# Kernel tuning notes

Hardware: AMD Instinct MI355X
Metric: run time of the kernel (lower is better)

Reference implementation:

```python
import jax, jax.numpy as jnp
import numpy as np

N, M = 4096, 8192
IN_DIM, OUT_DIM = 4096, 1024
NUM_SAMPLE = 10


def setup_inputs() -> dict:
    key = jax.random.key(0)
    k1, k2, k3, k4, k5 = jax.random.split(key, 5)
    node_features = jax.random.normal(k1, (N, IN_DIM), dtype=jnp.float32)
    neighbor_features = jax.random.normal(k2, (M, IN_DIM), dtype=jnp.float32)
    # Xavier-ish scale for params
    weight = jax.random.normal(k3, (OUT_DIM, IN_DIM), dtype=jnp.float32) * (1.0 / np.sqrt(IN_DIM))
    attention_vector = jax.random.normal(k4, (2 * OUT_DIM, 1), dtype=jnp.float32) * 0.05
    neighbor_idx = jax.random.randint(k5, (N, NUM_SAMPLE), 0, M, dtype=jnp.int32)
    return {
        "node_features": node_features,
        "neighbor_features": neighbor_features,
        "weight": weight,
        "attention_vector": attention_vector,
        "neighbor_idx": neighbor_idx,
    }


def reference(node_features, neighbor_features, weight, attention_vector, neighbor_idx):
    # Linear transform: [N, out], [M, out]
    node_t = node_features @ weight.T
    neigh_t = neighbor_features @ weight.T

    # combined @ attention_vector decomposes:
    # cat([h_i, h_j]) @ a == h_i @ a1 + h_j @ a2  (same math, no [N,M,2*out] tensor)
    a1 = attention_vector[:OUT_DIM, 0]   # [out]
    a2 = attention_vector[OUT_DIM:, 0]   # [out]
    scores = jax.nn.leaky_relu((node_t @ a1)[:, None] + (neigh_t @ a2)[None, :],
                               negative_slope=0.2)  # [N, M]

    # Build dense 0/1 mask from sampled neighbor indices (ragged -> dense)
    rows = jnp.arange(N, dtype=jnp.int32)[:, None]                  # [N,1]
    mask = jnp.zeros((N, M), dtype=jnp.float32).at[rows, neighbor_idx].set(1.0)

    scores = jnp.where(mask == 0, -jnp.inf, scores)
    attn = jax.nn.softmax(scores, axis=1)           # masked softmax over neighbor pool
    return attn @ neigh_t                           # [N, out]
```

## Files before the change

### kernel.cpp

```cpp
#include <hip/hip_runtime.h>

#define IN_DIM  4096
#define OUT_DIM 1024
#define NN      4096
#define MM      8192
#define NSAMP   10

typedef __bf16 bf16x8 __attribute__((ext_vector_type(8)));
typedef float  fx4    __attribute__((ext_vector_type(4)));

__device__ __forceinline__ ushort f2bf(float f) {
    union { float f; unsigned u; } v; v.f = f;
    unsigned u = v.u;
    return (ushort)((u + 0x7FFFu + ((u >> 16) & 1u)) >> 16);
}
__device__ __forceinline__ float bf2f(ushort u) {
    union { unsigned u; float f; } v; v.u = ((unsigned)u) << 16;
    return v.f;
}

#define GLDS(g, l) __builtin_amdgcn_global_load_lds(                           \
    (const __attribute__((address_space(1))) unsigned*)(g),                    \
    (__attribute__((address_space(3))) unsigned*)(l), 16, 0, 0)

__global__ __launch_bounds__(256) void k_attvec(const float* __restrict__ W,
                                                const float* __restrict__ att,
                                                float* __restrict__ v1,
                                                float* __restrict__ v2,
                                                ushort* __restrict__ Wbf) {
    int k  = blockIdx.x * 256 + threadIdx.x;
    int o0 = blockIdx.y * 32;
    float s1 = 0.f, s2 = 0.f;
    for (int o = o0; o < o0 + 32; ++o) {
        float w = W[(size_t)o * IN_DIM + k];
        Wbf[(size_t)o * IN_DIM + k] = f2bf(w);
        s1 += att[o] * w;
        s2 += att[OUT_DIM + o] * w;
    }
    atomicAdd(&v1[k], s1);
    atomicAdd(&v2[k], s2);
}

__global__ __launch_bounds__(256) void k_rows(const float* __restrict__ node_f,
                                              const float* __restrict__ neigh_f,
                                              const float* __restrict__ v1,
                                              const float* __restrict__ v2,
                                              float* __restrict__ nalpha,
                                              float* __restrict__ nbeta,
                                              ushort* __restrict__ Abf) {
    int row  = blockIdx.x * 4 + (threadIdx.x >> 6);
    int lane = threadIdx.x & 63;
    float s = 0.f;
    if (row < NN) {
        const float4* xr = reinterpret_cast<const float4*>(node_f + (size_t)row * IN_DIM);
        const float4* vr = reinterpret_cast<const float4*>(v1);
#pragma unroll
        for (int i = lane; i < IN_DIM / 4; i += 64) {
            float4 a = xr[i], b = vr[i];
            s += a.x * b.x + a.y * b.y + a.z * b.z + a.w * b.w;
        }
    } else {
        int j = row - NN;
        const float4* xr = reinterpret_cast<const float4*>(neigh_f + (size_t)j * IN_DIM);
        const float4* vr = reinterpret_cast<const float4*>(v2);
        ushort4* yr = reinterpret_cast<ushort4*>(Abf + (size_t)j * IN_DIM);
#pragma unroll
        for (int i = lane; i < IN_DIM / 4; i += 64) {
            float4 a = xr[i], b = vr[i];
            s += a.x * b.x + a.y * b.y + a.z * b.z + a.w * b.w;
            ushort4 o;
            o.x = f2bf(a.x); o.y = f2bf(a.y); o.z = f2bf(a.z); o.w = f2bf(a.w);
            yr[i] = o;
        }
    }
#pragma unroll
    for (int off = 32; off > 0; off >>= 1) s += __shfl_down(s, off, 64);
    if (lane == 0) {
        if (row < NN) nalpha[row] = s; else nbeta[row - NN] = s;
    }
}

#define BMT 256
#define BNT 256
#define BKG 32
#define KSPLIT (IN_DIM / 2)
#define NT (KSPLIT / BKG)

__device__ __forceinline__ void tile_compute(const ushort* __restrict__ as,
                                             const ushort* __restrict__ bs,
                                             int aoff, int boff,
                                             fx4 (&acc)[8][4]) {
    bf16x8 af[8], bfr[4];
#pragma unroll
    for (int mi = 0; mi < 8; ++mi)
        af[mi] = *reinterpret_cast<const bf16x8*>(as + aoff + mi * 512);
#pragma unroll
    for (int ni = 0; ni < 4; ++ni)
        bfr[ni] = *reinterpret_cast<const bf16x8*>(bs + boff + ni * 512);
    __builtin_amdgcn_s_setprio(1);
#pragma unroll
    for (int mi = 0; mi < 8; ++mi)
#pragma unroll
        for (int ni = 0; ni < 4; ++ni)
            acc[mi][ni] = __builtin_amdgcn_mfma_f32_16x16x32_bf16(af[mi], bfr[ni], acc[mi][ni], 0, 0, 0);
    __builtin_amdgcn_s_setprio(0);
}

__global__ __launch_bounds__(512, 2) void k_gemm(const ushort* __restrict__ A,
                                                 const ushort* __restrict__ B,
                                                 ushort* __restrict__ P) {
    __shared__ __align__(16) ushort As[4][BMT * BKG];
    __shared__ __align__(16) ushort Bs[4][BNT * BKG];

    const int tid  = threadIdx.x;
    const int lane = tid & 63;
    const int wid  = tid >> 6;
    const int wr   = wid >> 2;
    const int wc   = wid & 3;
    const int lrow = lane & 15;
    const int q    = lane >> 4;

    const int bid = blockIdx.x;
    const int swz = (bid & 7) * 32 + (bid >> 3);
    const int tx  = swz & 31;
    const int ty  = (swz >> 5) & 3;
    const int tz  = swz >> 7;
    const int bm  = tx * BMT;
    const int bn  = ty * BNT;
    const int kb  = tz * KSPLIT;

    const int sr  = tid >> 2;
    const int scu = (((tid & 3) ^ (sr & 3)) << 3);
    const ushort* gA0 = A + (size_t)(bm + sr) * IN_DIM + kb + scu;
    const ushort* gA1 = gA0 + (size_t)128 * IN_DIM;
    const ushort* gB0 = B + (size_t)(bn + sr) * IN_DIM + kb + scu;
    const ushort* gB1 = gB0 + (size_t)128 * IN_DIM;
    const int wbase = wid * 512;

#define STAGE(buf, kt) do {                                                    \
        GLDS(gA0 + (size_t)(kt) * BKG, &As[buf][0]        + wbase);            \
        GLDS(gA1 + (size_t)(kt) * BKG, &As[buf][0] + 4096 + wbase);            \
        GLDS(gB0 + (size_t)(kt) * BKG, &Bs[buf][0]        + wbase);            \
        GLDS(gB1 + (size_t)(kt) * BKG, &Bs[buf][0] + 4096 + wbase);            \
    } while (0)

    const int qs   = ((q ^ (lrow & 3)) << 3);
    const int aoff = (wr * 128 + lrow) * BKG + qs;
    const int boff = (wc * 64  + lrow) * BKG + qs;

    fx4 acc[8][4] = {};

    STAGE(0, 0); STAGE(1, 1); STAGE(2, 2);
    asm volatile("s_waitcnt vmcnt(8)" ::: "memory");
    __builtin_amdgcn_s_barrier();

    for (int t = 0; t < NT - 3; ++t) {
        STAGE((t + 3) & 3, t + 3);
        tile_compute(&As[t & 3][0], &Bs[t & 3][0], aoff, boff, acc);
        asm volatile("s_waitcnt vmcnt(8)" ::: "memory");
        __builtin_amdgcn_s_barrier();
    }
    tile_compute(&As[(NT - 3) & 3][0], &Bs[(NT - 3) & 3][0], aoff, boff, acc);
    asm volatile("s_waitcnt vmcnt(4)" ::: "memory");
    __builtin_amdgcn_s_barrier();
    tile_compute(&As[(NT - 2) & 3][0], &Bs[(NT - 2) & 3][0], aoff, boff, acc);
    asm volatile("s_waitcnt vmcnt(0)" ::: "memory");
    __builtin_amdgcn_s_barrier();
    tile_compute(&As[(NT - 1) & 3][0], &Bs[(NT - 1) & 3][0], aoff, boff, acc);
#undef STAGE

    ushort* Pz = P + (size_t)tz * MM * OUT_DIM;
#pragma unroll
    for (int mi = 0; mi < 8; ++mi)
#pragma unroll
        for (int ni = 0; ni < 4; ++ni) {
            int r = bm + wr * 128 + mi * 16 + q * 4;
            int c = bn + wc * 64  + ni * 16 + lrow;
#pragma unroll
            for (int v = 0; v < 4; ++v)
                Pz[(size_t)(r + v) * OUT_DIM + c] = f2bf(acc[mi][ni][v]);
        }
}

__global__ __launch_bounds__(256) void k_aggregate(const ushort* __restrict__ P,
                                                   const float* __restrict__ nalpha,
                                                   const float* __restrict__ nbeta,
                                                   const int* __restrict__ nidx,
                                                   float* __restrict__ outp) {
    int row = blockIdx.x;
    __shared__ int   s_idx[NSAMP];
    __shared__ float s_w[NSAMP];
    if (threadIdx.x < 16) {
        int t = threadIdx.x;
        int j = (t < NSAMP) ? nidx[row * NSAMP + t] : -1;
        float score = -INFINITY;
        if (t < NSAMP) {
            float x = nalpha[row] + nbeta[j];
            score = x > 0.f ? x : 0.2f * x;
        }
        bool dup = false;
#pragma unroll
        for (int sIdx = 0; sIdx < NSAMP; ++sIdx) {
            int js = __shfl(j, sIdx, 16);
            if (sIdx < t && js == j) dup = true;
        }
        float mx = score;
#pragma unroll
        for (int off = 8; off > 0; off >>= 1) {
            float o = __shfl_xor(mx, off, 16);
            mx = o > mx ? o : mx;
        }
        float e = (t < NSAMP && !dup) ? expf(score - mx) : 0.f;
        float sum = e;
#pragma unroll
        for (int off = 8; off > 0; off >>= 1) sum += __shfl_xor(sum, off, 16);
        if (t < NSAMP) {
            s_idx[t] = j;
            s_w[t]   = e / sum;
        }
    }
    __syncthreads();
    int col = threadIdx.x * 4;
    float ax = 0.f, ay = 0.f, az = 0.f, aw = 0.f;
#pragma unroll
    for (int t = 0; t < NSAMP; ++t) {
        float w = s_w[t];
        size_t off = (size_t)s_idx[t] * OUT_DIM + col;
        ushort4 u0 = *reinterpret_cast<const ushort4*>(P + off);
        ushort4 u1 = *reinterpret_cast<const ushort4*>(P + (size_t)MM * OUT_DIM + off);
        ax += w * (bf2f(u0.x) + bf2f(u1.x));
        ay += w * (bf2f(u0.y) + bf2f(u1.y));
        az += w * (bf2f(u0.z) + bf2f(u1.z));
        aw += w * (bf2f(u0.w) + bf2f(u1.w));
    }
    float4 o; o.x = ax; o.y = ay; o.z = az; o.w = aw;
    *reinterpret_cast<float4*>(outp + (size_t)row * OUT_DIM + col) = o;
}

extern "C" void kernel_launch(void* const* d_in, const int* in_sizes, int n_in,
                              void* d_out, int out_size, void* d_ws, size_t ws_size,
                              hipStream_t stream) {
    const float* node_f  = (const float*)d_in[0];
    const float* neigh_f = (const float*)d_in[1];
    const float* W       = (const float*)d_in[2];
    const float* att     = (const float*)d_in[3];
    const int*   nidx    = (const int*)d_in[4];
    float* outp = (float*)d_out;

    char* ws = (char*)d_ws;
    ushort* Abf = (ushort*)ws;
    ushort* Wbf = (ushort*)(ws + 67108864);
    ushort* P   = (ushort*)(ws + 75497472);
    float*  v1     = (float*)(ws + 109051904);
    float*  v2     = v1 + IN_DIM;
    float*  nalpha = v2 + IN_DIM;
    float*  nbeta  = nalpha + NN;

    hipMemsetAsync(v1, 0, 2 * IN_DIM * sizeof(float), stream);

    k_attvec   <<<dim3(16, 32),   256, 0, stream>>>(W, att, v1, v2, Wbf);
    k_rows     <<<(NN + MM) / 4,  256, 0, stream>>>(node_f, neigh_f, v1, v2, nalpha, nbeta, Abf);
    k_gemm     <<<256,            512, 0, stream>>>(Abf, Wbf, P);
    k_aggregate<<<NN,             256, 0, stream>>>(P, nalpha, nbeta, nidx, outp);
}
```

Measured before the change: 410.0 us.

## Restructure GEMM main loop into split-phase ping-pong with interleaved staging

The GEMM main loop now uses prefetch distance two instead of three. Each k-tile is split into two half-phases separated by barriers, and the A and B global-to-LDS loads for tile t+2 are interleaved with the MFMA halves. The LDS XOR swizzle changes to use bits 1-2 of the row, to cut bank conflicts on the fragment reads. k_attvec gets twice as many blocks, each with a 16-row unrolled loop, for more parallelism. The extra barriers and shallower prefetch could expose memory latency in exchange for lower register pressure and better overlap.

```diff
diff --git a/kernel.cpp b/kernel.cpp
--- a/kernel.cpp
+++ b/kernel.cpp
@@ -22,6 +22,8 @@
 #define GLDS(g, l) __builtin_amdgcn_global_load_lds(                           \
     (const __attribute__((address_space(1))) unsigned*)(g),                    \
     (__attribute__((address_space(3))) unsigned*)(l), 16, 0, 0)
+
+#define VMWAIT(N) asm volatile("s_waitcnt vmcnt(" #N ")" ::: "memory")
 
 __global__ __launch_bounds__(256) void k_attvec(const float* __restrict__ W,
                                                 const float* __restrict__ att,
@@ -29,9 +31,10 @@
                                                 float* __restrict__ v2,
                                                 ushort* __restrict__ Wbf) {
     int k  = blockIdx.x * 256 + threadIdx.x;
-    int o0 = blockIdx.y * 32;
+    int o0 = blockIdx.y * 16;
     float s1 = 0.f, s2 = 0.f;
-    for (int o = o0; o < o0 + 32; ++o) {
+#pragma unroll
+    for (int o = o0; o < o0 + 16; ++o) {
         float w = W[(size_t)o * IN_DIM + k];
         Wbf[(size_t)o * IN_DIM + k] = f2bf(w);
         s1 += att[o] * w;
@@ -86,25 +89,7 @@
 #define KSPLIT (IN_DIM / 2)
 #define NT (KSPLIT / BKG)
 
-__device__ __forceinline__ void tile_compute(const ushort* __restrict__ as,
-                                             const ushort* __restrict__ bs,
-                                             int aoff, int boff,
-                                             fx4 (&acc)[8][4]) {
-    bf16x8 af[8], bfr[4];
-#pragma unroll
-    for (int mi = 0; mi < 8; ++mi)
-        af[mi] = *reinterpret_cast<const bf16x8*>(as + aoff + mi * 512);
-#pragma unroll
-    for (int ni = 0; ni < 4; ++ni)
-        bfr[ni] = *reinterpret_cast<const bf16x8*>(bs + boff + ni * 512);
-    __builtin_amdgcn_s_setprio(1);
-#pragma unroll
-    for (int mi = 0; mi < 8; ++mi)
-#pragma unroll
-        for (int ni = 0; ni < 4; ++ni)
-            acc[mi][ni] = __builtin_amdgcn_mfma_f32_16x16x32_bf16(af[mi], bfr[ni], acc[mi][ni], 0, 0, 0);
-    __builtin_amdgcn_s_setprio(0);
-}
+#define MF(x, y, mi, ni) acc[mi][ni] = __builtin_amdgcn_mfma_f32_16x16x32_bf16((x), (y), acc[mi][ni], 0, 0, 0)
 
 __global__ __launch_bounds__(512, 2) void k_gemm(const ushort* __restrict__ A,
                                                  const ushort* __restrict__ B,
@@ -130,44 +115,88 @@
     const int kb  = tz * KSPLIT;
 
     const int sr  = tid >> 2;
-    const int scu = (((tid & 3) ^ (sr & 3)) << 3);
+    const int scu = (((tid & 3) ^ ((sr >> 1) & 3)) << 3);
     const ushort* gA0 = A + (size_t)(bm + sr) * IN_DIM + kb + scu;
     const ushort* gA1 = gA0 + (size_t)128 * IN_DIM;
     const ushort* gB0 = B + (size_t)(bn + sr) * IN_DIM + kb + scu;
     const ushort* gB1 = gB0 + (size_t)128 * IN_DIM;
     const int wbase = wid * 512;
 
-#define STAGE(buf, kt) do {                                                    \
+#define STAGE_FULL(buf, kt) do {                                               \
         GLDS(gA0 + (size_t)(kt) * BKG, &As[buf][0]        + wbase);            \
         GLDS(gA1 + (size_t)(kt) * BKG, &As[buf][0] + 4096 + wbase);            \
         GLDS(gB0 + (size_t)(kt) * BKG, &Bs[buf][0]        + wbase);            \
         GLDS(gB1 + (size_t)(kt) * BKG, &Bs[buf][0] + 4096 + wbase);            \
     } while (0)
 
-    const int qs   = ((q ^ (lrow & 3)) << 3);
+    const int qs   = ((q ^ ((lrow >> 1) & 3)) << 3);
     const int aoff = (wr * 128 + lrow) * BKG + qs;
     const int boff = (wc * 64  + lrow) * BKG + qs;
 
     fx4 acc[8][4] = {};
 
-    STAGE(0, 0); STAGE(1, 1); STAGE(2, 2);
-    asm volatile("s_waitcnt vmcnt(8)" ::: "memory");
+    STAGE_FULL(0, 0);
+    STAGE_FULL(1, 1);
+    VMWAIT(4);
     __builtin_amdgcn_s_barrier();
-
-    for (int t = 0; t < NT - 3; ++t) {
-        STAGE((t + 3) & 3, t + 3);
-        tile_compute(&As[t & 3][0], &Bs[t & 3][0], aoff, boff, acc);
-        asm volatile("s_waitcnt vmcnt(8)" ::: "memory");
-        __builtin_amdgcn_s_barrier();
-    }
-    tile_compute(&As[(NT - 3) & 3][0], &Bs[(NT - 3) & 3][0], aoff, boff, acc);
-    asm volatile("s_waitcnt vmcnt(4)" ::: "memory");
-    __builtin_amdgcn_s_barrier();
-    tile_compute(&As[(NT - 2) & 3][0], &Bs[(NT - 2) & 3][0], aoff, boff, acc);
-    asm volatile("s_waitcnt vmcnt(0)" ::: "memory");
-    __builtin_amdgcn_s_barrier();
-    tile_compute(&As[(NT - 1) & 3][0], &Bs[(NT - 1) & 3][0], aoff, boff, acc);
-#undef STAGE
+    asm volatile("" ::: "memory");
+
+#define TILE_BODY(t_, STG_, WAITK_) do {                                       \
+        const int bt_ = (t_) & 3;                                              \
+        const ushort* as_ = &As[bt_][0];                                       \
+        const ushort* bs_ = &Bs[bt_][0];                                       \
+        bf16x8 a0, a1, a2, a3, b0, b1, b2, b3;                                 \
+        a0 = *reinterpret_cast<const bf16x8*>(as_ + aoff + 0 * 512);           \
+        a1 = *reinterpret_cast<const bf16x8*>(as_ + aoff + 1 * 512);           \
+        a2 = *reinterpret_cast<const bf16x8*>(as_ + aoff + 2 * 512);           \
+        a3 = *reinterpret_cast<const bf16x8*>(as_ + aoff + 3 * 512);           \
+        b0 = *reinterpret_cast<const bf16x8*>(bs_ + boff + 0 * 512);           \
+        b1 = *reinterpret_cast<const bf16x8*>(bs_ + boff + 1 * 512);           \
+        b2 = *reinterpret_cast<const bf16x8*>(bs_ + boff + 2 * 512);           \
+        b3 = *reinterpret_cast<const bf16x8*>(bs_ + boff + 3 * 512);           \
+        if (STG_) {                                                            \
+            ushort* d_ = &As[((t_) + 2) & 3][0] + wbase;                       \
+            GLDS(gA0 + (size_t)((t_) + 2) * BKG, d_);                         \
+            GLDS(gA1 + (size_t)((t_) + 2) * BKG, d_ + 4096);                  \
+        }                                                                      \
+        __builtin_amdgcn_s_barrier();                                          \
+        asm volatile("" ::: "memory");                                         \
+        __builtin_amdgcn_s_setprio(1);                                         \
+        MF(a0, b0, 0, 0); MF(a0, b1, 0, 1); MF(a0, b2, 0, 2); MF(a0, b3, 0, 3);\
+        MF(a1, b0, 1, 0); MF(a1, b1, 1, 1); MF(a1, b2, 1, 2); MF(a1, b3, 1, 3);\
+        MF(a2, b0, 2, 0); MF(a2, b1, 2, 1); MF(a2, b2, 2, 2); MF(a2, b3, 2, 3);\
+        MF(a3, b0, 3, 0); MF(a3, b1, 3, 1); MF(a3, b2, 3, 2); MF(a3, b3, 3, 3);\
+        __builtin_amdgcn_s_setprio(0);                                         \
+        __builtin_amdgcn_s_barrier();                                          \
+        asm volatile("" ::: "memory");                                         \
+        a0 = *reinterpret_cast<const bf16x8*>(as_ + aoff + 4 * 512);           \
+        a1 = *reinterpret_cast<const bf16x8*>(as_ + aoff + 5 * 512);           \
+        a2 = *reinterpret_cast<const bf16x8*>(as_ + aoff + 6 * 512);           \
+        a3 = *reinterpret_cast<const bf16x8*>(as_ + aoff + 7 * 512);           \
+        if (STG_) {                                                            \
+            ushort* d_ = &Bs[((t_) + 2) & 3][0] + wbase;                       \
+            GLDS(gB0 + (size_t)((t_) + 2) * BKG, d_);                         \
+            GLDS(gB1 + (size_t)((t_) + 2) * BKG, d_ + 4096);                  \
+        }                                                                      \
+        if ((WAITK_) == 0) { VMWAIT(4); } else if ((WAITK_) == 1) { VMWAIT(0); }\
+        __builtin_amdgcn_s_barrier();                                          \
+        asm volatile("" ::: "memory");                                         \
+        __builtin_amdgcn_s_setprio(1);                                         \
+        MF(a0, b0, 4, 0); MF(a0, b1, 4, 1); MF(a0, b2, 4, 2); MF(a0, b3, 4, 3);\
+        MF(a1, b0, 5, 0); MF(a1, b1, 5, 1); MF(a1, b2, 5, 2); MF(a1, b3, 5, 3);\
+        MF(a2, b0, 6, 0); MF(a2, b1, 6, 1); MF(a2, b2, 6, 2); MF(a2, b3, 6, 3);\
+        MF(a3, b0, 7, 0); MF(a3, b1, 7, 1); MF(a3, b2, 7, 2); MF(a3, b3, 7, 3);\
+        __builtin_amdgcn_s_setprio(0);                                         \
+        __builtin_amdgcn_s_barrier();                                          \
+        asm volatile("" ::: "memory");                                         \
+    } while (0)
+
+    for (int t = 0; t < NT - 2; ++t)
+        TILE_BODY(t, 1, 0);
+    TILE_BODY(NT - 2, 0, 1);
+    TILE_BODY(NT - 1, 0, 2);
+#undef TILE_BODY
+#undef STAGE_FULL
 
     ushort* Pz = P + (size_t)tz * MM * OUT_DIM;
 #pragma unroll
@@ -258,7 +287,7 @@
 
     hipMemsetAsync(v1, 0, 2 * IN_DIM * sizeof(float), stream);
 
-    k_attvec   <<<dim3(16, 32),   256, 0, stream>>>(W, att, v1, v2, Wbf);
+    k_attvec   <<<dim3(16, 64),   256, 0, stream>>>(W, att, v1, v2, Wbf);
     k_rows     <<<(NN + MM) / 4,  256, 0, stream>>>(node_f, neigh_f, v1, v2, nalpha, nbeta, Abf);
     k_gemm     <<<256,            512, 0, stream>>>(Abf, Wbf, P);
     k_aggregate<<<NN,             256, 0, stream>>>(P, nalpha, nbeta, nidx, outp);
```

Result: no change. 406.1 us (-1.0%).
